# Performance work log

Hardware: AMD Instinct MI355X
Metric: run time of the kernel (lower is better)

The kernel has to match this reference:

```python
import jax, jax.numpy as jnp
import numpy as np

B, T, I, H, L = 32, 512, 512, 512, 2


def _gru_layer(x, w_ih, w_hh, b_ih, b_hh, reverse):
    # x: [B, T, in] ; w_ih: [3H, in] ; w_hh: [3H, H] ; gate order (r, z, n) as in PyTorch
    Bh = x.shape[0]
    Hh = w_hh.shape[1]
    pre = jnp.einsum('bti,gi->btg', x, w_ih) + b_ih  # [B, T, 3H] input projections, done once
    if reverse:
        pre = pre[:, ::-1]
    pre_t = jnp.swapaxes(pre, 0, 1)  # [T, B, 3H]
    h0 = jnp.zeros((Bh, Hh), x.dtype)

    def step(h, gx):
        gh = h @ w_hh.T + b_hh  # [B, 3H]
        r = jax.nn.sigmoid(gx[:, :Hh] + gh[:, :Hh])
        z = jax.nn.sigmoid(gx[:, Hh:2 * Hh] + gh[:, Hh:2 * Hh])
        n = jnp.tanh(gx[:, 2 * Hh:] + r * gh[:, 2 * Hh:])
        h_new = (1.0 - z) * n + z * h
        return h_new, h_new

    h_last, ys = jax.lax.scan(step, h0, pre_t)
    ys = jnp.swapaxes(ys, 0, 1)  # [B, T, H]
    if reverse:
        ys = ys[:, ::-1]
    return ys, h_last


def _encoder(context, params):
    # params: list of (w_ih, w_hh, b_ih, b_hh, w_ih_r, w_hh_r, b_ih_r, b_hh_r) per layer
    x = context
    finals = []  # interleaved fwd, bwd per layer, like torch GRU's `final`
    for (w_ih, w_hh, b_ih, b_hh, w_ih_r, w_hh_r, b_ih_r, b_hh_r) in params:
        y_f, h_f = _gru_layer(x, w_ih, w_hh, b_ih, b_hh, reverse=False)
        y_b, h_b = _gru_layer(x, w_ih_r, w_hh_r, b_ih_r, b_hh_r, reverse=True)
        x = jnp.concatenate([y_f, y_b], axis=-1)  # [B, T, 2H]
        finals.append(h_f)
        finals.append(h_b)
    final = jnp.stack(finals, axis=0)  # [2L, B, H]
    fwd_final = final[0::2]  # [L, B, H]
    bwd_final = final[1::2]
    final = jnp.concatenate([fwd_final, bwd_final], axis=2)  # [L, B, 2H]
    return x, final


def setup_inputs() -> dict:
    key = jax.random.key(0)
    ks = jax.random.split(key, 20)
    s = 1.0 / np.sqrt(H)  # PyTorch-style uniform-ish scale
    d = {'context': jax.random.normal(ks[0], (B, T, I), jnp.float32)}
    shapes = {
        'w_ih_l0': (3 * H, I), 'w_hh_l0': (3 * H, H), 'b_ih_l0': (3 * H,), 'b_hh_l0': (3 * H,),
        'w_ih_l0r': (3 * H, I), 'w_hh_l0r': (3 * H, H), 'b_ih_l0r': (3 * H,), 'b_hh_l0r': (3 * H,),
        'w_ih_l1': (3 * H, 2 * H), 'w_hh_l1': (3 * H, H), 'b_ih_l1': (3 * H,), 'b_hh_l1': (3 * H,),
        'w_ih_l1r': (3 * H, 2 * H), 'w_hh_l1r': (3 * H, H), 'b_ih_l1r': (3 * H,), 'b_hh_l1r': (3 * H,),
    }
    for i, (name, shp) in enumerate(shapes.items()):
        d[name] = jax.random.normal(ks[i + 1], shp, jnp.float32) * s
    return d


def reference(context, w_ih_l0, w_hh_l0, b_ih_l0, b_hh_l0,
              w_ih_l0r, w_hh_l0r, b_ih_l0r, b_hh_l0r,
              w_ih_l1, w_hh_l1, b_ih_l1, b_hh_l1,
              w_ih_l1r, w_hh_l1r, b_ih_l1r, b_hh_l1r):
    params = [
        (w_ih_l0, w_hh_l0, b_ih_l0, b_hh_l0, w_ih_l0r, w_hh_l0r, b_ih_l0r, b_hh_l0r),
        (w_ih_l1, w_hh_l1, b_ih_l1, b_hh_l1, w_ih_l1r, w_hh_l1r, b_ih_l1r, b_hh_l1r),
    ]
    return _encoder(context, params)
```

## Files before the change

### kernel.cpp

```cpp
#include <hip/hip_runtime.h>

typedef unsigned int  u32;
typedef unsigned short u16;
typedef short s16x8 __attribute__((ext_vector_type(8)));
typedef float f32x4 __attribute__((ext_vector_type(4)));

#define BB 32
#define TT 512
#define HH 512
#define GG 1536
#define MM 16384

__device__ __forceinline__ u16 f2bf(float f) {
  u32 u = __builtin_bit_cast(u32, f);
  u = u + 0x7FFFu + ((u >> 16) & 1u);
  return (u16)(u >> 16);
}
__device__ __forceinline__ float bf2f(u16 h) {
  return __builtin_bit_cast(float, (u32)h << 16);
}
__device__ __forceinline__ float sigmoidf_(float x) { return 1.f / (1.f + __expf(-x)); }
__device__ __forceinline__ float tanhf_(float x)    { return 1.f - 2.f / (__expf(2.f * x) + 1.f); }


struct PrepP {
  const float *ctx;
  const float *wih0, *whh0, *bih0, *bhh0, *wih0r, *whh0r, *bih0r, *bhh0r;
  const float *wih1, *whh1, *bih1, *bhh1, *wih1r, *whh1r, *bih1r, *bhh1r;
  u16 *a0f, *w0f, *w1f, *whh;
  float *bgx, *bhn;
  u32 *ctr;
};

__global__ void prep_kernel(PrepP P) {
  const size_t NA0 = (size_t)MM * 512;
  const size_t NW0 = (size_t)3072 * 512;
  const size_t NW1 = (size_t)3072 * 1024;
  const size_t NWH = (size_t)2 * 2 * GG * HH;
  const size_t NBG = 2 * 2 * (size_t)GG;
  const size_t NBN = 2 * 2 * (size_t)HH;
  const size_t TOTAL = NA0 + NW0 + NW1 + NWH + NBG + NBN + 4;
  size_t stride = (size_t)gridDim.x * blockDim.x;
  for (size_t i = (size_t)blockIdx.x * blockDim.x + threadIdx.x; i < TOTAL; i += stride) {
    size_t e = i;
    if (e < NA0) {
      int j = e & 7, l = (e >> 3) & 63, kb = (e >> 9) & 15, mb = (int)(e >> 13);
      int m = mb * 16 + (l & 15);
      int k = kb * 32 + ((l >> 4) << 2) + (j & 3) + ((j >> 2) << 4);
      P.a0f[e] = f2bf(P.ctx[(size_t)m * 512 + k]);
      continue;
    }
    e -= NA0;
    if (e < NW0) {
      int j = e & 7, l = (e >> 3) & 63, kb = (e >> 9) & 15, nb = (int)(e >> 13);
      int n = nb * 16 + (l & 15);
      int d = (n >= GG) ? 1 : 0, g = n - d * GG;
      int k = kb * 32 + ((l >> 4) << 2) + (j & 3) + ((j >> 2) << 4);
      const float* src = d ? P.wih0r : P.wih0;
      P.w0f[e] = f2bf(src[(size_t)g * 512 + k]);
      continue;
    }
    e -= NW0;
    if (e < NW1) {
      int j = e & 7, l = (e >> 3) & 63, kb = (e >> 9) & 31, nb = (int)(e >> 14);
      int n = nb * 16 + (l & 15);
      int d = (n >= GG) ? 1 : 0, g = n - d * GG;
      int k = kb * 32 + ((l >> 4) << 2) + (j & 3) + ((j >> 2) << 4);
      const float* src = d ? P.wih1r : P.wih1;
      P.w1f[e] = f2bf(src[(size_t)g * 1024 + k]);
      continue;
    }
    e -= NW1;
    if (e < NWH) {
      size_t per = (size_t)GG * HH;
      int ld = (int)(e / per); size_t sub = e % per;
      const float* src = (ld == 0) ? P.whh0 : (ld == 1) ? P.whh0r : (ld == 2) ? P.whh1 : P.whh1r;
      P.whh[e] = f2bf(src[sub]);
      continue;
    }
    e -= NWH;
    if (e < NBG) {
      int ld = (int)(e / GG), g = (int)(e % GG);
      const float* bi = (ld == 0) ? P.bih0 : (ld == 1) ? P.bih0r : (ld == 2) ? P.bih1 : P.bih1r;
      const float* bh = (ld == 0) ? P.bhh0 : (ld == 1) ? P.bhh0r : (ld == 2) ? P.bhh1 : P.bhh1r;
      P.bgx[e] = bi[g] + ((g < 1024) ? bh[g] : 0.f);
      continue;
    }
    e -= NBG;
    if (e < NBN) {
      int ld = (int)(e / HH), u = (int)(e % HH);
      const float* bh = (ld == 0) ? P.bhh0 : (ld == 1) ? P.bhh0r : (ld == 2) ? P.bhh1 : P.bhh1r;
      P.bhn[e] = bh[1024 + u];
      continue;
    }
    e -= NBN;
    if (e < 4) P.ctr[e] = 0u;
  }
}

template<bool GXF32>
__global__ __launch_bounds__(256, 2) void proj_kernel(const u16* __restrict__ A,
                                                      const u16* __restrict__ W,
                                                      void* __restrict__ gx, int KB) {
  __shared__ uint4 As4[512];
  __shared__ uint4 Bs4[512];
  const int tid = threadIdx.x;
  const int bm = blockIdx.x, bn = blockIdx.y;
  const int l = tid & 63, w = tid >> 6, wm = w >> 1, wn = w & 1;

  f32x4 acc[4][4];
#pragma unroll
  for (int i = 0; i < 4; ++i)
#pragma unroll
    for (int j = 0; j < 4; ++j) acc[i][j] = f32x4{0.f, 0.f, 0.f, 0.f};

  const uint4* GA = (const uint4*)A;
  const uint4* GB = (const uint4*)W;

  for (int kt = 0; kt < KB; ++kt) {
    __syncthreads();
#pragma unroll
    for (int c = 0; c < 2; ++c) {
      int idx = tid * 2 + c;
      int blk = idx >> 6, pos = idx & 63;
      As4[idx] = GA[((size_t)(bm * 8 + blk) * KB + kt) * 64 + pos];
      Bs4[idx] = GB[((size_t)(bn * 8 + blk) * KB + kt) * 64 + pos];
    }
    __syncthreads();
    s16x8 av[4], bv[4];
#pragma unroll
    for (int mf = 0; mf < 4; ++mf) av[mf] = ((const s16x8*)As4)[(wm * 4 + mf) * 64 + l];
#pragma unroll
    for (int nf = 0; nf < 4; ++nf) bv[nf] = ((const s16x8*)Bs4)[(wn * 4 + nf) * 64 + l];
#pragma unroll
    for (int mf = 0; mf < 4; ++mf)
#pragma unroll
      for (int nf = 0; nf < 4; ++nf)
        acc[mf][nf] = __builtin_amdgcn_mfma_f32_16x16x32_bf16(av[mf], bv[nf], acc[mf][nf], 0, 0, 0);
  }

#pragma unroll
  for (int mf = 0; mf < 4; ++mf)
#pragma unroll
    for (int nf = 0; nf < 4; ++nf)
#pragma unroll
      for (int r = 0; r < 4; ++r) {
        int m = bm * 128 + wm * 64 + mf * 16 + (l >> 4) * 4 + r;
        int n = bn * 128 + wn * 64 + nf * 16 + (l & 15);
        int b = m >> 9, t = m & 511;
        int d = (n >= GG) ? 1 : 0, g = n - d * GG;
        size_t o = ((size_t)(d * TT + t) * BB + b) * GG + g;
        float v = acc[mf][nf][r];
        if (GXF32) ((float*)gx)[o] = v;
        else       ((u16*)gx)[o] = f2bf(v);
      }
}

template<bool GXF32, bool YF32>
__global__ __launch_bounds__(256, 1) void recur_kernel(
    const void* __restrict__ gx_, const u16* __restrict__ whh,
    const float* __restrict__ bgx, const float* __restrict__ bhn_,
    void* __restrict__ yout, float* __restrict__ finals,
    u16* __restrict__ hex, u32* __restrict__ ctr) {
  const int wg = blockIdx.x, d = wg >> 4, s = wg & 15;
  const int tid = threadIdx.x, l = tid & 63, w = tid >> 6;
  const int nt = w & 1, uh = w >> 1;
  const int l4 = l >> 4, lm = l & 15;
  const int b = nt * 16 + lm;
  const int u0 = s * 32 + uh * 16 + l4 * 4;

  s16x8 af[3][16];
  const u16* wd = whh + (size_t)d * (GG * HH);
#pragma unroll
  for (int g = 0; g < 3; ++g) {
    const int row = g * 512 + s * 32 + uh * 16 + lm;
    const u16* rp = wd + (size_t)row * 512 + l4 * 4;
#pragma unroll
    for (int ks = 0; ks < 16; ++ks) {
      uint2 lo = *(const uint2*)(rp + ks * 32);
      uint2 hi = *(const uint2*)(rp + ks * 32 + 16);
      uint4 t4; t4.x = lo.x; t4.y = lo.y; t4.z = hi.x; t4.w = hi.y;
      af[g][ks] = __builtin_bit_cast(s16x8, t4);
    }
  }
  float bgr[4], bgz[4], bgn[4], bhn[4];
#pragma unroll
  for (int r = 0; r < 4; ++r) {
    bgr[r] = bgx[d * GG + 0 * 512 + u0 + r];
    bgz[r] = bgx[d * GG + 1 * 512 + u0 + r];
    bgn[r] = bgx[d * GG + 2 * 512 + u0 + r];
    bhn[r] = bhn_[d * HH + u0 + r];
  }
  float h[4] = {0.f, 0.f, 0.f, 0.f};
  u32* c = ctr + d;

  const u32 HEXB = 65536;
  const u32 wbyte = (u32)(((((d * 16 + s) * 2 + nt) * 64 + l) * 8 + 4 * uh) * 2);
  const u32 rbyte = (u32)((((d * 16) * 2 + nt) * 64 + l) * 8 * 2);

  {
    uint2 z; z.x = 0u; z.y = 0u;
    asm volatile("global_store_dwordx2 %0, %1, %2 sc0 sc1"
                 :: "v"(wbyte), "v"(z), "s"(hex) : "memory");
    asm volatile("s_waitcnt vmcnt(0)" ::: "memory");
    __syncthreads();
    if (tid == 0)
      __hip_atomic_fetch_add(c, 1u, __ATOMIC_RELAXED, __HIP_MEMORY_SCOPE_AGENT);
  }

  float gxr[4], gxz[4], gxn[4];
  {
    const int t0 = d ? 511 : 0;
    const size_t base = ((size_t)(d * TT + t0) * BB + b) * GG + u0;
    if (GXF32) {
      const float* Gp = (const float*)gx_ + base;
      f32x4 vr = *(const f32x4*)(Gp);
      f32x4 vz = *(const f32x4*)(Gp + 512);
      f32x4 vn = *(const f32x4*)(Gp + 1024);
#pragma unroll
      for (int r = 0; r < 4; ++r) { gxr[r] = vr[r]; gxz[r] = vz[r]; gxn[r] = vn[r]; }
    } else {
      const u16* Gp = (const u16*)gx_ + base;
      uint2 vr = *(const uint2*)(Gp);
      uint2 vz = *(const uint2*)(Gp + 512);
      uint2 vn = *(const uint2*)(Gp + 1024);
      gxr[0] = bf2f((u16)vr.x); gxr[1] = bf2f((u16)(vr.x >> 16)); gxr[2] = bf2f((u16)vr.y); gxr[3] = bf2f((u16)(vr.y >> 16));
      gxz[0] = bf2f((u16)vz.x); gxz[1] = bf2f((u16)(vz.x >> 16)); gxz[2] = bf2f((u16)vz.y); gxz[3] = bf2f((u16)(vz.y >> 16));
      gxn[0] = bf2f((u16)vn.x); gxn[1] = bf2f((u16)(vn.x >> 16)); gxn[2] = bf2f((u16)vn.y); gxn[3] = bf2f((u16)(vn.y >> 16));
    }
  }

  if (l == 0) {
    while (__hip_atomic_load(c, __ATOMIC_RELAXED, __HIP_MEMORY_SCOPE_AGENT) < 16u) {}
  }

  for (int sig = 0; sig < 512; ++sig) {
    const int t = d ? (511 - sig) : sig;

    const u32 ro = (u32)(sig & 1) * HEXB + rbyte;
    uint4 bfr[16];
#pragma unroll
    for (int ks = 0; ks < 16; ++ks)
      asm volatile("global_load_dwordx4 %0, %1, %2 sc0 sc1"
                   : "=v"(bfr[ks]) : "v"(ro + ks * 2048), "s"(hex) : "memory");

    f32x4 a0 = {0.f, 0.f, 0.f, 0.f}, a1 = a0, a2 = a0;
    asm volatile("s_waitcnt vmcnt(8)" ::: "memory");
    __builtin_amdgcn_sched_barrier(0);
#pragma unroll
    for (int ks = 0; ks < 8; ++ks) {
      s16x8 bfv = __builtin_bit_cast(s16x8, bfr[ks]);
      a0 = __builtin_amdgcn_mfma_f32_16x16x32_bf16(af[0][ks], bfv, a0, 0, 0, 0);
      a1 = __builtin_amdgcn_mfma_f32_16x16x32_bf16(af[1][ks], bfv, a1, 0, 0, 0);
      a2 = __builtin_amdgcn_mfma_f32_16x16x32_bf16(af[2][ks], bfv, a2, 0, 0, 0);
    }
    asm volatile("s_waitcnt vmcnt(0)" ::: "memory");
    __builtin_amdgcn_sched_barrier(0);
#pragma unroll
    for (int ks = 8; ks < 16; ++ks) {
      s16x8 bfv = __builtin_bit_cast(s16x8, bfr[ks]);
      a0 = __builtin_amdgcn_mfma_f32_16x16x32_bf16(af[0][ks], bfv, a0, 0, 0, 0);
      a1 = __builtin_amdgcn_mfma_f32_16x16x32_bf16(af[1][ks], bfv, a1, 0, 0, 0);
      a2 = __builtin_amdgcn_mfma_f32_16x16x32_bf16(af[2][ks], bfv, a2, 0, 0, 0);
    }

    u16 hb16[4];
#pragma unroll
    for (int r = 0; r < 4; ++r) {
      float rr = sigmoidf_(gxr[r] + bgr[r] + a0[r]);
      float zz = sigmoidf_(gxz[r] + bgz[r] + a1[r]);
      float nn = tanhf_(gxn[r] + bgn[r] + rr * (a2[r] + bhn[r]));
      h[r] = (1.f - zz) * nn + zz * h[r];
      hb16[r] = f2bf(h[r]);
    }
    uint2 pk; pk.x = (u32)hb16[0] | ((u32)hb16[1] << 16); pk.y = (u32)hb16[2] | ((u32)hb16[3] << 16);

    if (sig < 511) {
      const u32 wo = (u32)((sig + 1) & 1) * HEXB + wbyte;
      asm volatile("global_store_dwordx2 %0, %1, %2 sc0 sc1"
                   :: "v"(wo), "v"(pk), "s"(hex) : "memory");
      asm volatile("s_waitcnt vmcnt(0)" ::: "memory");
      __syncthreads();
      if (tid == 0)
        __hip_atomic_fetch_add(c, 1u, __ATOMIC_RELAXED, __HIP_MEMORY_SCOPE_AGENT);
    }

    if (YF32) {
      float4 yv; yv.x = h[0]; yv.y = h[1]; yv.z = h[2]; yv.w = h[3];
      *(float4*)((float*)yout + ((size_t)(b * TT + t) * 1024 + d * 512 + u0)) = yv;
    } else {
      size_t o = (((size_t)(b * 32 + (t >> 4)) * 32 + (d * 16 + s)) * 64 + (l4 * 16 + (t & 15))) * 8 + 4 * uh;
      *(uint2*)((u16*)yout + o) = pk;
    }
    if (sig == 511) {
      float4 fv; fv.x = h[0]; fv.y = h[1]; fv.z = h[2]; fv.w = h[3];
      *(float4*)(finals + (size_t)b * 1024 + d * 512 + u0) = fv;
      break;
    }
    {
      const int t2 = d ? (511 - (sig + 1)) : (sig + 1);
      const size_t base = ((size_t)(d * TT + t2) * BB + b) * GG + u0;
      if (GXF32) {
        const float* Gp = (const float*)gx_ + base;
        f32x4 vr = *(const f32x4*)(Gp);
        f32x4 vz = *(const f32x4*)(Gp + 512);
        f32x4 vn = *(const f32x4*)(Gp + 1024);
#pragma unroll
        for (int r = 0; r < 4; ++r) { gxr[r] = vr[r]; gxz[r] = vz[r]; gxn[r] = vn[r]; }
      } else {
        const u16* Gp = (const u16*)gx_ + base;
        uint2 vr = *(const uint2*)(Gp);
        uint2 vz = *(const uint2*)(Gp + 512);
        uint2 vn = *(const uint2*)(Gp + 1024);
        gxr[0] = bf2f((u16)vr.x); gxr[1] = bf2f((u16)(vr.x >> 16)); gxr[2] = bf2f((u16)vr.y); gxr[3] = bf2f((u16)(vr.y >> 16));
        gxz[0] = bf2f((u16)vz.x); gxz[1] = bf2f((u16)(vz.x >> 16)); gxz[2] = bf2f((u16)vz.y); gxz[3] = bf2f((u16)(vz.y >> 16));
        gxn[0] = bf2f((u16)vn.x); gxn[1] = bf2f((u16)(vn.x >> 16)); gxn[2] = bf2f((u16)vn.y); gxn[3] = bf2f((u16)(vn.y >> 16));
      }
    }

    if (l == 0) {
      const u32 tgt = 16u * (u32)(sig + 2);
      while (__hip_atomic_load(c, __ATOMIC_RELAXED, __HIP_MEMORY_SCOPE_AGENT) < tgt) {}
    }
  }
}

extern "C" void kernel_launch(void* const* d_in, const int* in_sizes, int n_in,
                              void* d_out, int out_size, void* d_ws, size_t ws_size,
                              hipStream_t stream) {
  (void)in_sizes; (void)n_in; (void)out_size;
  const float* ctx   = (const float*)d_in[0];
  const float* wih0  = (const float*)d_in[1];
  const float* whh0  = (const float*)d_in[2];
  const float* bih0  = (const float*)d_in[3];
  const float* bhh0  = (const float*)d_in[4];
  const float* wih0r = (const float*)d_in[5];
  const float* whh0r = (const float*)d_in[6];
  const float* bih0r = (const float*)d_in[7];
  const float* bhh0r = (const float*)d_in[8];
  const float* wih1  = (const float*)d_in[9];
  const float* whh1  = (const float*)d_in[10];
  const float* bih1  = (const float*)d_in[11];
  const float* bhh1  = (const float*)d_in[12];
  const float* wih1r = (const float*)d_in[13];
  const float* whh1r = (const float*)d_in[14];
  const float* bih1r = (const float*)d_in[15];
  const float* bhh1r = (const float*)d_in[16];

  char* ws = (char*)d_ws;
  size_t off = 0;
  auto take = [&](size_t bytes) { char* p = ws + off; off += bytes; return p; };
  u16*   a0f  = (u16*)take(16777216);
  u16*   a1f  = (u16*)take(33554432);
  u16*   w0f  = (u16*)take(3145728);
  u16*   w1f  = (u16*)take(6291456);
  u16*   whhb = (u16*)take(6291456);
  float* bgx  = (float*)take(24576);
  float* bhn  = (float*)take(8192);
  u32*   ctr  = (u32*)take(256);
  u16*   hex  = (u16*)take(131072);
  const size_t GXF32_BYTES = 201326592;
  const size_t GXB16_BYTES = 100663296;
  bool gxf32 = (ws_size >= off + GXF32_BYTES);
  void* gx = (void*)take(gxf32 ? GXF32_BYTES : GXB16_BYTES);

  PrepP P;
  P.ctx = ctx;
  P.wih0 = wih0; P.whh0 = whh0; P.bih0 = bih0; P.bhh0 = bhh0;
  P.wih0r = wih0r; P.whh0r = whh0r; P.bih0r = bih0r; P.bhh0r = bhh0r;
  P.wih1 = wih1; P.whh1 = whh1; P.bih1 = bih1; P.bhh1 = bhh1;
  P.wih1r = wih1r; P.whh1r = whh1r; P.bih1r = bih1r; P.bhh1r = bhh1r;
  P.a0f = a0f; P.w0f = w0f; P.w1f = w1f; P.whh = whhb;
  P.bgx = bgx; P.bhn = bhn; P.ctr = ctr;

  prep_kernel<<<dim3(2048), dim3(256), 0, stream>>>(P);

  float* fin = (float*)d_out + (size_t)MM * 1024;
  if (gxf32) {
    proj_kernel<true><<<dim3(128, 24), dim3(256), 0, stream>>>(a0f, w0f, gx, 16);
    recur_kernel<true, false><<<dim3(32), dim3(256), 0, stream>>>(
        gx, whhb, bgx, bhn, a1f, fin, hex, ctr);
    proj_kernel<true><<<dim3(128, 24), dim3(256), 0, stream>>>(a1f, w1f, gx, 32);
    recur_kernel<true, true><<<dim3(32), dim3(256), 0, stream>>>(
        gx, whhb + (size_t)2 * GG * HH, bgx + 2 * GG, bhn + 2 * HH, d_out, fin + 32768, hex, ctr + 2);
  } else {
    proj_kernel<false><<<dim3(128, 24), dim3(256), 0, stream>>>(a0f, w0f, gx, 16);
    recur_kernel<false, false><<<dim3(32), dim3(256), 0, stream>>>(
        gx, whhb, bgx, bhn, a1f, fin, hex, ctr);
    proj_kernel<false><<<dim3(128, 24), dim3(256), 0, stream>>>(a1f, w1f, gx, 32);
    recur_kernel<false, true><<<dim3(32), dim3(256), 0, stream>>>(
        gx, whhb + (size_t)2 * GG * HH, bgx + 2 * GG, bhn + 2 * HH, d_out, fin + 32768, hex, ctr + 2);
  }
}
```

Baseline: 3.550 ms.

## Replace per-step atomic counter barrier with per-wave flag polling

Drops the shared atomic counter and the __syncthreads in the recurrent loop. Each wave now publishes its own step number into a flag array, and consumers poll all 64 flags of their direction with a wave-wide __all before loading the hidden state. Step 0 skips the matmul because h starts at zero, and each layer gets its own exchange buffer and flag region. This is meant to cut barrier latency and atomic contention on the serial critical path. The cost is heavier polling traffic and finer-grained memory-ordering assumptions.

```diff
diff --git a/kernel.cpp b/kernel.cpp
--- a/kernel.cpp
+++ b/kernel.cpp
@@ -4,6 +4,8 @@
 typedef unsigned short u16;
 typedef short s16x8 __attribute__((ext_vector_type(8)));
 typedef float f32x4 __attribute__((ext_vector_type(4)));
+typedef u32 u32x2 __attribute__((ext_vector_type(2)));
+typedef u32 u32x4 __attribute__((ext_vector_type(4)));
 
 #define BB 32
 #define TT 512
@@ -29,7 +31,7 @@
   const float *wih1, *whh1, *bih1, *bhh1, *wih1r, *whh1r, *bih1r, *bhh1r;
   u16 *a0f, *w0f, *w1f, *whh;
   float *bgx, *bhn;
-  u32 *ctr;
+  u32 *flg;
 };
 
 __global__ void prep_kernel(PrepP P) {
@@ -39,7 +41,8 @@
   const size_t NWH = (size_t)2 * 2 * GG * HH;
   const size_t NBG = 2 * 2 * (size_t)GG;
   const size_t NBN = 2 * 2 * (size_t)HH;
-  const size_t TOTAL = NA0 + NW0 + NW1 + NWH + NBG + NBN + 4;
+  const size_t NFL = 256;
+  const size_t TOTAL = NA0 + NW0 + NW1 + NWH + NBG + NBN + NFL;
   size_t stride = (size_t)gridDim.x * blockDim.x;
   for (size_t i = (size_t)blockIdx.x * blockDim.x + threadIdx.x; i < TOTAL; i += stride) {
     size_t e = i;
@@ -94,7 +97,7 @@
       continue;
     }
     e -= NBN;
-    if (e < 4) P.ctr[e] = 0u;
+    if (e < NFL) { P.flg[e] = 0u; continue; }
   }
 }
 
@@ -156,12 +159,23 @@
       }
 }
 
+__device__ __forceinline__ u32x4 hld16(const u16* p, u32 off) {
+  u32x4 r;
+  asm volatile("global_load_dwordx4 %0, %1, %2 sc0 sc1"
+               : "=v"(r) : "v"(off), "s"(p) : "memory");
+  return r;
+}
+__device__ __forceinline__ void hst8(u16* p, u32 off, u32x2 v) {
+  asm volatile("global_store_dwordx2 %0, %1, %2 sc0 sc1"
+               :: "v"(off), "v"(v), "s"(p) : "memory");
+}
+
 template<bool GXF32, bool YF32>
 __global__ __launch_bounds__(256, 1) void recur_kernel(
     const void* __restrict__ gx_, const u16* __restrict__ whh,
     const float* __restrict__ bgx, const float* __restrict__ bhn_,
     void* __restrict__ yout, float* __restrict__ finals,
-    u16* __restrict__ hex, u32* __restrict__ ctr) {
+    u16* __restrict__ hex, u32* __restrict__ flg) {
   const int wg = blockIdx.x, d = wg >> 4, s = wg & 15;
   const int tid = threadIdx.x, l = tid & 63, w = tid >> 6;
   const int nt = w & 1, uh = w >> 1;
@@ -177,9 +191,11 @@
     const u16* rp = wd + (size_t)row * 512 + l4 * 4;
 #pragma unroll
     for (int ks = 0; ks < 16; ++ks) {
-      uint2 lo = *(const uint2*)(rp + ks * 32);
-      uint2 hi = *(const uint2*)(rp + ks * 32 + 16);
-      uint4 t4; t4.x = lo.x; t4.y = lo.y; t4.z = hi.x; t4.w = hi.y;
+      u32 lo0 = *(const u32*)(rp + ks * 32);
+      u32 lo1 = *(const u32*)(rp + ks * 32 + 2);
+      u32 hi0 = *(const u32*)(rp + ks * 32 + 16);
+      u32 hi1 = *(const u32*)(rp + ks * 32 + 18);
+      u32x4 t4; t4.x = lo0; t4.y = lo1; t4.z = hi0; t4.w = hi1;
       af[g][ks] = __builtin_bit_cast(s16x8, t4);
     }
   }
@@ -192,21 +208,12 @@
     bhn[r] = bhn_[d * HH + u0 + r];
   }
   float h[4] = {0.f, 0.f, 0.f, 0.f};
-  u32* c = ctr + d;
 
   const u32 HEXB = 65536;
   const u32 wbyte = (u32)(((((d * 16 + s) * 2 + nt) * 64 + l) * 8 + 4 * uh) * 2);
-  const u32 rbyte = (u32)((((d * 16) * 2 + nt) * 64 + l) * 8 * 2);
-
-  {
-    uint2 z; z.x = 0u; z.y = 0u;
-    asm volatile("global_store_dwordx2 %0, %1, %2 sc0 sc1"
-                 :: "v"(wbyte), "v"(z), "s"(hex) : "memory");
-    asm volatile("s_waitcnt vmcnt(0)" ::: "memory");
-    __syncthreads();
-    if (tid == 0)
-      __hip_atomic_fetch_add(c, 1u, __ATOMIC_RELAXED, __HIP_MEMORY_SCOPE_AGENT);
-  }
+  const u32 rbyte = (u32)(((d * 32 + nt) * 64 + l) * 16);
+  u32* fdir = flg + d * 64;
+  const int fw = s * 4 + w;
 
   float gxr[4], gxz[4], gxn[4];
   {
@@ -220,48 +227,48 @@
 #pragma unroll
       for (int r = 0; r < 4; ++r) { gxr[r] = vr[r]; gxz[r] = vz[r]; gxn[r] = vn[r]; }
     } else {
-      const u16* Gp = (const u16*)gx_ + base;
-      uint2 vr = *(const uint2*)(Gp);
-      uint2 vz = *(const uint2*)(Gp + 512);
-      uint2 vn = *(const uint2*)(Gp + 1024);
-      gxr[0] = bf2f((u16)vr.x); gxr[1] = bf2f((u16)(vr.x >> 16)); gxr[2] = bf2f((u16)vr.y); gxr[3] = bf2f((u16)(vr.y >> 16));
-      gxz[0] = bf2f((u16)vz.x); gxz[1] = bf2f((u16)(vz.x >> 16)); gxz[2] = bf2f((u16)vz.y); gxz[3] = bf2f((u16)(vz.y >> 16));
-      gxn[0] = bf2f((u16)vn.x); gxn[1] = bf2f((u16)(vn.x >> 16)); gxn[2] = bf2f((u16)vn.y); gxn[3] = bf2f((u16)(vn.y >> 16));
-    }
-  }
-
-  if (l == 0) {
-    while (__hip_atomic_load(c, __ATOMIC_RELAXED, __HIP_MEMORY_SCOPE_AGENT) < 16u) {}
+      const u32* Gp = (const u32*)((const u16*)gx_ + base);
+      u32 vr0 = Gp[0], vr1 = Gp[1], vz0 = Gp[256], vz1 = Gp[257], vn0 = Gp[512], vn1 = Gp[513];
+      gxr[0] = bf2f((u16)vr0); gxr[1] = bf2f((u16)(vr0 >> 16)); gxr[2] = bf2f((u16)vr1); gxr[3] = bf2f((u16)(vr1 >> 16));
+      gxz[0] = bf2f((u16)vz0); gxz[1] = bf2f((u16)(vz0 >> 16)); gxz[2] = bf2f((u16)vz1); gxz[3] = bf2f((u16)(vz1 >> 16));
+      gxn[0] = bf2f((u16)vn0); gxn[1] = bf2f((u16)(vn0 >> 16)); gxn[2] = bf2f((u16)vn1); gxn[3] = bf2f((u16)(vn1 >> 16));
+    }
   }
 
   for (int sig = 0; sig < 512; ++sig) {
     const int t = d ? (511 - sig) : sig;
 
-    const u32 ro = (u32)(sig & 1) * HEXB + rbyte;
-    uint4 bfr[16];
-#pragma unroll
-    for (int ks = 0; ks < 16; ++ks)
-      asm volatile("global_load_dwordx4 %0, %1, %2 sc0 sc1"
-                   : "=v"(bfr[ks]) : "v"(ro + ks * 2048), "s"(hex) : "memory");
-
     f32x4 a0 = {0.f, 0.f, 0.f, 0.f}, a1 = a0, a2 = a0;
-    asm volatile("s_waitcnt vmcnt(8)" ::: "memory");
-    __builtin_amdgcn_sched_barrier(0);
-#pragma unroll
-    for (int ks = 0; ks < 8; ++ks) {
-      s16x8 bfv = __builtin_bit_cast(s16x8, bfr[ks]);
-      a0 = __builtin_amdgcn_mfma_f32_16x16x32_bf16(af[0][ks], bfv, a0, 0, 0, 0);
-      a1 = __builtin_amdgcn_mfma_f32_16x16x32_bf16(af[1][ks], bfv, a1, 0, 0, 0);
-      a2 = __builtin_amdgcn_mfma_f32_16x16x32_bf16(af[2][ks], bfv, a2, 0, 0, 0);
-    }
-    asm volatile("s_waitcnt vmcnt(0)" ::: "memory");
-    __builtin_amdgcn_sched_barrier(0);
-#pragma unroll
-    for (int ks = 8; ks < 16; ++ks) {
-      s16x8 bfv = __builtin_bit_cast(s16x8, bfr[ks]);
-      a0 = __builtin_amdgcn_mfma_f32_16x16x32_bf16(af[0][ks], bfv, a0, 0, 0, 0);
-      a1 = __builtin_amdgcn_mfma_f32_16x16x32_bf16(af[1][ks], bfv, a1, 0, 0, 0);
-      a2 = __builtin_amdgcn_mfma_f32_16x16x32_bf16(af[2][ks], bfv, a2, 0, 0, 0);
+    if (sig > 0) {
+      u32 v;
+      do {
+        v = __hip_atomic_load(fdir + l, __ATOMIC_RELAXED, __HIP_MEMORY_SCOPE_AGENT);
+      } while (!__all((int)v >= sig));
+
+      const u32 ro = (u32)(sig & 1) * HEXB + rbyte;
+      u32x4 bfr[16];
+#pragma unroll
+      for (int ks = 0; ks < 16; ++ks)
+        bfr[ks] = hld16(hex, ro + (u32)ks * 2048);
+
+      asm volatile("s_waitcnt vmcnt(8)" ::: "memory");
+      __builtin_amdgcn_sched_barrier(0);
+#pragma unroll
+      for (int ks = 0; ks < 8; ++ks) {
+        s16x8 bv = __builtin_bit_cast(s16x8, bfr[ks]);
+        a0 = __builtin_amdgcn_mfma_f32_16x16x32_bf16(af[0][ks], bv, a0, 0, 0, 0);
+        a1 = __builtin_amdgcn_mfma_f32_16x16x32_bf16(af[1][ks], bv, a1, 0, 0, 0);
+        a2 = __builtin_amdgcn_mfma_f32_16x16x32_bf16(af[2][ks], bv, a2, 0, 0, 0);
+      }
+      asm volatile("s_waitcnt vmcnt(0)" ::: "memory");
+      __builtin_amdgcn_sched_barrier(0);
+#pragma unroll
+      for (int ks = 8; ks < 16; ++ks) {
+        s16x8 bv = __builtin_bit_cast(s16x8, bfr[ks]);
+        a0 = __builtin_amdgcn_mfma_f32_16x16x32_bf16(af[0][ks], bv, a0, 0, 0, 0);
+        a1 = __builtin_amdgcn_mfma_f32_16x16x32_bf16(af[1][ks], bv, a1, 0, 0, 0);
+        a2 = __builtin_amdgcn_mfma_f32_16x16x32_bf16(af[2][ks], bv, a2, 0, 0, 0);
+      }
     }
 
     u16 hb16[4];
@@ -273,30 +280,28 @@
       h[r] = (1.f - zz) * nn + zz * h[r];
       hb16[r] = f2bf(h[r]);
     }
-    uint2 pk; pk.x = (u32)hb16[0] | ((u32)hb16[1] << 16); pk.y = (u32)hb16[2] | ((u32)hb16[3] << 16);
+    u32x2 pk; pk.x = (u32)hb16[0] | ((u32)hb16[1] << 16); pk.y = (u32)hb16[2] | ((u32)hb16[3] << 16);
 
     if (sig < 511) {
-      const u32 wo = (u32)((sig + 1) & 1) * HEXB + wbyte;
-      asm volatile("global_store_dwordx2 %0, %1, %2 sc0 sc1"
-                   :: "v"(wo), "v"(pk), "s"(hex) : "memory");
+      hst8(hex, (u32)((sig + 1) & 1) * HEXB + wbyte, pk);
       asm volatile("s_waitcnt vmcnt(0)" ::: "memory");
-      __syncthreads();
-      if (tid == 0)
-        __hip_atomic_fetch_add(c, 1u, __ATOMIC_RELAXED, __HIP_MEMORY_SCOPE_AGENT);
+      if (l == 0)
+        __hip_atomic_store(fdir + fw, (u32)(sig + 1), __ATOMIC_RELAXED, __HIP_MEMORY_SCOPE_AGENT);
     }
 
     if (YF32) {
-      float4 yv; yv.x = h[0]; yv.y = h[1]; yv.z = h[2]; yv.w = h[3];
-      *(float4*)((float*)yout + ((size_t)(b * TT + t) * 1024 + d * 512 + u0)) = yv;
+      f32x4 yv; yv.x = h[0]; yv.y = h[1]; yv.z = h[2]; yv.w = h[3];
+      *(f32x4*)((float*)yout + ((size_t)(b * TT + t) * 1024 + d * 512 + u0)) = yv;
     } else {
       size_t o = (((size_t)(b * 32 + (t >> 4)) * 32 + (d * 16 + s)) * 64 + (l4 * 16 + (t & 15))) * 8 + 4 * uh;
-      *(uint2*)((u16*)yout + o) = pk;
+      *(u32x2*)((u16*)yout + o) = pk;
     }
     if (sig == 511) {
-      float4 fv; fv.x = h[0]; fv.y = h[1]; fv.z = h[2]; fv.w = h[3];
-      *(float4*)(finals + (size_t)b * 1024 + d * 512 + u0) = fv;
+      f32x4 fv; fv.x = h[0]; fv.y = h[1]; fv.z = h[2]; fv.w = h[3];
+      *(f32x4*)(finals + (size_t)b * 1024 + d * 512 + u0) = fv;
       break;
     }
+
     {
       const int t2 = d ? (511 - (sig + 1)) : (sig + 1);
       const size_t base = ((size_t)(d * TT + t2) * BB + b) * GG + u0;
@@ -308,19 +313,12 @@
 #pragma unroll
         for (int r = 0; r < 4; ++r) { gxr[r] = vr[r]; gxz[r] = vz[r]; gxn[r] = vn[r]; }
       } else {
-        const u16* Gp = (const u16*)gx_ + base;
-        uint2 vr = *(const uint2*)(Gp);
-        uint2 vz = *(const uint2*)(Gp + 512);
-        uint2 vn = *(const uint2*)(Gp + 1024);
-        gxr[0] = bf2f((u16)vr.x); gxr[1] = bf2f((u16)(vr.x >> 16)); gxr[2] = bf2f((u16)vr.y); gxr[3] = bf2f((u16)(vr.y >> 16));
-        gxz[0] = bf2f((u16)vz.x); gxz[1] = bf2f((u16)(vz.x >> 16)); gxz[2] = bf2f((u16)vz.y); gxz[3] = bf2f((u16)(vz.y >> 16));
-        gxn[0] = bf2f((u16)vn.x); gxn[1] = bf2f((u16)(vn.x >> 16)); gxn[2] = bf2f((u16)vn.y); gxn[3] = bf2f((u16)(vn.y >> 16));
+        const u32* Gp = (const u32*)((const u16*)gx_ + base);
+        u32 vr0 = Gp[0], vr1 = Gp[1], vz0 = Gp[256], vz1 = Gp[257], vn0 = Gp[512], vn1 = Gp[513];
+        gxr[0] = bf2f((u16)vr0); gxr[1] = bf2f((u16)(vr0 >> 16)); gxr[2] = bf2f((u16)vr1); gxr[3] = bf2f((u16)(vr1 >> 16));
+        gxz[0] = bf2f((u16)vz0); gxz[1] = bf2f((u16)(vz0 >> 16)); gxz[2] = bf2f((u16)vz1); gxz[3] = bf2f((u16)(vz1 >> 16));
+        gxn[0] = bf2f((u16)vn0); gxn[1] = bf2f((u16)(vn0 >> 16)); gxn[2] = bf2f((u16)vn1); gxn[3] = bf2f((u16)(vn1 >> 16));
       }
-    }
-
-    if (l == 0) {
-      const u32 tgt = 16u * (u32)(sig + 2);
-      while (__hip_atomic_load(c, __ATOMIC_RELAXED, __HIP_MEMORY_SCOPE_AGENT) < tgt) {}
     }
   }
 }
@@ -357,8 +355,9 @@
   u16*   whhb = (u16*)take(6291456);
   float* bgx  = (float*)take(24576);
   float* bhn  = (float*)take(8192);
-  u32*   ctr  = (u32*)take(256);
-  u16*   hex  = (u16*)take(131072);
+  u32*   flg  = (u32*)take(1024);
+  u16*   hexA = (u16*)take(131072);
+  u16*   hexB = (u16*)take(131072);
   const size_t GXF32_BYTES = 201326592;
   const size_t GXB16_BYTES = 100663296;
   bool gxf32 = (ws_size >= off + GXF32_BYTES);
@@ -371,7 +370,7 @@
   P.wih1 = wih1; P.whh1 = whh1; P.bih1 = bih1; P.bhh1 = bhh1;
   P.wih1r = wih1r; P.whh1r = whh1r; P.bih1r = bih1r; P.bhh1r = bhh1r;
   P.a0f = a0f; P.w0f = w0f; P.w1f = w1f; P.whh = whhb;
-  P.bgx = bgx; P.bhn = bhn; P.ctr = ctr;
+  P.bgx = bgx; P.bhn = bhn; P.flg = flg;
 
   prep_kernel<<<dim3(2048), dim3(256), 0, stream>>>(P);
 
@@ -379,16 +378,18 @@
   if (gxf32) {
     proj_kernel<true><<<dim3(128, 24), dim3(256), 0, stream>>>(a0f, w0f, gx, 16);
     recur_kernel<true, false><<<dim3(32), dim3(256), 0, stream>>>(
-        gx, whhb, bgx, bhn, a1f, fin, hex, ctr);
+        gx, whhb, bgx, bhn, a1f, fin, hexA, flg);
     proj_kernel<true><<<dim3(128, 24), dim3(256), 0, stream>>>(a1f, w1f, gx, 32);
     recur_kernel<true, true><<<dim3(32), dim3(256), 0, stream>>>(
-        gx, whhb + (size_t)2 * GG * HH, bgx + 2 * GG, bhn + 2 * HH, d_out, fin + 32768, hex, ctr + 2);
+        gx, whhb + (size_t)2 * GG * HH, bgx + 2 * GG, bhn + 2 * HH, d_out, fin + 32768,
+        hexB, flg + 128);
   } else {
     proj_kernel<false><<<dim3(128, 24), dim3(256), 0, stream>>>(a0f, w0f, gx, 16);
     recur_kernel<false, false><<<dim3(32), dim3(256), 0, stream>>>(
-        gx, whhb, bgx, bhn, a1f, fin, hex, ctr);
+        gx, whhb, bgx, bhn, a1f, fin, hexA, flg);
     proj_kernel<false><<<dim3(128, 24), dim3(256), 0, stream>>>(a1f, w1f, gx, 32);
     recur_kernel<false, true><<<dim3(32), dim3(256), 0, stream>>>(
-        gx, whhb + (size_t)2 * GG * HH, bgx + 2 * GG, bhn + 2 * HH, d_out, fin + 32768, hex, ctr + 2);
-  }
-}
+        gx, whhb + (size_t)2 * GG * HH, bgx + 2 * GG, bhn + 2 * HH, d_out, fin + 32768,
+        hexB, flg + 128);
+  }
+}
```

New measurement: 3.323 ms. 1.07x faster.
